# Optimization experiments

Hardware: AMD Instinct MI355X
Metric: run time of the kernel (lower is better)

The kernel has to match this reference:

```python
import jax, jax.numpy as jnp
import numpy as np

S, B, I, H = 2048, 4096, 2, 6  # seq, batch, input_size, hidden_size


def setup_inputs() -> dict:
    key = jax.random.key(0)
    ks = jax.random.split(key, 11)
    init = lambda k, sh: jax.random.normal(k, sh, dtype=jnp.float32) * 0.1
    return {
        "x": jax.random.normal(ks[0], (S, B, I), dtype=jnp.float32),
        # layer-0 LSTM params (PyTorch gate order: i, f, g, o)
        "Wih0": init(ks[1], (4 * H, I)),
        "Whh0": init(ks[2], (4 * H, H)),
        "bih0": init(ks[3], (4 * H,)),
        "bhh0": init(ks[4], (4 * H,)),
        # layer-1 LSTM params
        "Wih1": init(ks[5], (4 * H, H)),
        "Whh1": init(ks[6], (4 * H, H)),
        "bih1": init(ks[7], (4 * H,)),
        "bhh1": init(ks[8], (4 * H,)),
        # final Linear(6, 1)
        "W2": init(ks[9], (1, H)),
        "b2": init(ks[10], (1,)),
    }


def _lstm_layer(x, Wih, Whh, bih, bhh):
    # x: (S, B, in_dim) -> hidden outputs (S, B, H)
    Bn = x.shape[1]
    Hn = Whh.shape[1]
    b = bih + bhh
    # precompute input projections for all timesteps at once (memory-bound GEMM)
    xg = jnp.einsum("sbi,gi->sbg", x, Wih) + b  # (S, B, 4H)

    def step(carry, xt_g):
        h, c = carry
        g = xt_g + h @ Whh.T  # (B, 4H)
        i, f, gg, o = jnp.split(g, 4, axis=-1)
        i = jax.nn.sigmoid(i)
        f = jax.nn.sigmoid(f)
        gg = jnp.tanh(gg)
        o = jax.nn.sigmoid(o)
        c = f * c + i * gg
        h = o * jnp.tanh(c)
        return (h, c), h

    h0 = jnp.zeros((Bn, Hn), dtype=x.dtype)
    c0 = jnp.zeros((Bn, Hn), dtype=x.dtype)
    _, hs = jax.lax.scan(step, (h0, c0), xg)
    return hs  # (S, B, H)


def reference(x, Wih0, Whh0, bih0, bhh0, Wih1, Whh1, bih1, bhh1, W2, b2):
    h1 = _lstm_layer(x, Wih0, Whh0, bih0, bhh0)   # (S, B, H)
    h2 = _lstm_layer(h1, Wih1, Whh1, bih1, bhh1)  # (S, B, H); dropout disabled (eval)
    flat = h2.reshape(-1, H)                       # (S*B, H)
    out = flat @ W2.T + b2                         # (S*B, 1) — original discards final view
    return out
```

## Files before the change

### kernel.cpp

```cpp
#include <hip/hip_runtime.h>

#define SEQ   2048
#define BATCH 4096
#define HID   6
#define BLK   256

typedef float v2f __attribute__((ext_vector_type(2)));
typedef unsigned u2 __attribute__((ext_vector_type(2)));

__device__ __forceinline__ float fexp2(float a) {
#if __has_builtin(__builtin_amdgcn_exp2f)
  return __builtin_amdgcn_exp2f(a);
#else
  float r; asm("v_exp_f32 %0, %1" : "=v"(r) : "v"(a)); return r;
#endif
}
__device__ __forceinline__ float frcp(float a) {
#if __has_builtin(__builtin_amdgcn_rcpf)
  return __builtin_amdgcn_rcpf(a);
#else
  float r; asm("v_rcp_f32 %0, %1" : "=v"(r) : "v"(a)); return r;
#endif
}

template <int CTRL>
__device__ __forceinline__ float dppf(float v) {
  int r = __builtin_amdgcn_update_dpp(0, __builtin_bit_cast(int, v), CTRL, 0xF, 0xF, true);
  return __builtin_bit_cast(float, r);
}

__device__ __forceinline__ float xhalf(float v, bool hi) {
#if __has_builtin(__builtin_amdgcn_permlane32_swap)
  u2 r = __builtin_amdgcn_permlane32_swap(__builtin_bit_cast(unsigned, v),
                                          __builtin_bit_cast(unsigned, v), false, false);
  return __builtin_bit_cast(float, hi ? r.x : r.y);
#else
  unsigned d = __builtin_bit_cast(unsigned, v), s = d;
  asm volatile("v_permlane32_swap_b32 %0, %1" : "+v"(d), "+v"(s));
  return __builtin_bit_cast(float, hi ? d : s);
#endif
}

__global__ __launch_bounds__(BLK, 1) void lstm2_kernel(
    const float* __restrict__ x,
    const float* __restrict__ Wih0, const float* __restrict__ Whh0,
    const float* __restrict__ bih0, const float* __restrict__ bhh0,
    const float* __restrict__ Wih1, const float* __restrict__ Whh1,
    const float* __restrict__ bih1, const float* __restrict__ bhh1,
    const float* __restrict__ W2,   const float* __restrict__ b2,
    float* __restrict__ out)
{
  __shared__ float obuf[64][16];

  const int tid = threadIdx.x;
  const int wib = tid >> 6;
  const int l6  = tid & 63;
  const bool hi = l6 >= 32;
  const int j   = l6 & 31;
  const int el  = j >> 3;
  const int u   = j & 7;
  const int uu  = (u < HID) ? u : (HID - 1);
  const int b   = blockIdx.x * 16 + wib * 4 + el;

  v2f WA[4][4], WB[4][4], w2r[4];
  float BS[4];
#pragma unroll
  for (int q = 0; q < 4; ++q) {
    const int rq = q * HID + uu;
    const float Kq = (q == 2) ? -2.8853900817779268f : -1.4426950408889634f;
#pragma unroll
    for (int k = 0; k < 4; ++k) {
      const int k0 = u ^ (2 * k), k1 = u ^ (2 * k + 1);
      const bool ok0 = (k0 < HID), ok1 = (k1 < HID);
      if (!hi) {
        WA[q][k] = v2f{0.f, 0.f};
        WB[q][k] = v2f{ok0 ? Kq * Whh0[rq * HID + k0] : 0.f,
                       ok1 ? Kq * Whh0[rq * HID + k1] : 0.f};
      } else {
        WA[q][k] = v2f{ok0 ? Kq * Wih1[rq * HID + k0] : 0.f,
                       ok1 ? Kq * Wih1[rq * HID + k1] : 0.f};
        WB[q][k] = v2f{ok0 ? Kq * Whh1[rq * HID + k0] : 0.f,
                       ok1 ? Kq * Whh1[rq * HID + k1] : 0.f};
      }
    }
    if (!hi) WA[q][0] = v2f{Kq * Wih0[rq * 2 + 0], Kq * Wih0[rq * 2 + 1]};
    BS[q] = Kq * ((!hi ? bih0[rq] : bih1[rq]) + (!hi ? bhh0[rq] : bhh1[rq]));
  }
#pragma unroll
  for (int k = 0; k < 4; ++k) {
    const int k0 = u ^ (2 * k), k1 = u ^ (2 * k + 1);
    w2r[k] = v2f{(k0 < HID) ? W2[k0] : 0.f, (k1 < HID) ? W2[k1] : 0.f};
  }
  const float bout = b2[0];
  const float KT = 2.8853900817779268f;

  float h = 0.f, c = 0.f;

  auto gath = [&](float hv, v2f (&g)[4]) {
    float t1 = dppf<0xB1>(hv);
    float t2 = dppf<0x4E>(hv);
    float t3 = dppf<0x4E>(t1);
    float m  = dppf<0x141>(hv);
    float m1 = dppf<0xB1>(m);
    float m2 = dppf<0x4E>(m);
    float m3 = dppf<0x4E>(m1);
    g[0] = v2f{hv, t1};
    g[1] = v2f{t2, t3};
    g[2] = v2f{m3, m2};
    g[3] = v2f{m1, m};
  };

  auto step = [&](v2f xc, float& ov) {
    v2f g2[4]; gath(h, g2);
    float hs = xhalf(h, hi);
    v2f g1[4]; gath(hs, g1);
    v2f v10 = hi ? g1[0] : xc;

    float a[4];
#pragma unroll
    for (int q = 0; q < 4; ++q) {
      v2f accA = __builtin_elementwise_fma(WA[q][0], v10, v2f{BS[q], 0.f});
      accA = __builtin_elementwise_fma(WA[q][1], g1[1], accA);
      accA = __builtin_elementwise_fma(WA[q][2], g1[2], accA);
      accA = __builtin_elementwise_fma(WA[q][3], g1[3], accA);
      v2f accB = WB[q][0] * g2[0];
      accB = __builtin_elementwise_fma(WB[q][1], g2[1], accB);
      accB = __builtin_elementwise_fma(WB[q][2], g2[2], accB);
      accB = __builtin_elementwise_fma(WB[q][3], g2[3], accB);
      v2f acc = accA + accB;
      a[q] = acc.x + acc.y;
    }
    v2f ao = __builtin_elementwise_fma(w2r[0], g2[0],
             __builtin_elementwise_fma(w2r[1], g2[1],
             __builtin_elementwise_fma(w2r[2], g2[2],
             __builtin_elementwise_fma(w2r[3], g2[3], v2f{bout, 0.f}))));
    ov = ao.x + ao.y;

    float i_ = frcp(1.f + fexp2(a[0]));
    float f_ = frcp(1.f + fexp2(a[1]));
    float g_ = fmaf(2.f, frcp(1.f + fexp2(a[2])), -1.f);
    float o_ = frcp(1.f + fexp2(a[3]));
    c = fmaf(f_, c, i_ * g_);
    float th = fmaf(-2.f, frcp(1.f + fexp2(c * KT)), 1.f);
    h = o_ * th;
  };

  auto flush = [&](int rbase) {
    const int r = tid >> 2, jj = (tid & 3) * 4;
    float4 vv = *(const float4*)&obuf[r][jj];
    *(float4*)&out[(size_t)(rbase + r) * BATCH + blockIdx.x * 16 + jj] = vv;
  };

  const v2f* x2 = (const v2f*)x;
  v2f xc  = x2[(size_t)0 * BATCH + b];
  v2f xn1 = x2[(size_t)1 * BATCH + b];
  v2f xn2 = x2[(size_t)2 * BATCH + b];
  v2f xn3 = x2[(size_t)3 * BATCH + b];

  {
    float ov;
    step(xc, ov);
    if (hi) { h = 0.f; c = 0.f; }
    v2f xf = x2[(size_t)4 * BATCH + b];
    xc = xn1; xn1 = xn2; xn2 = xn3; xn3 = xf;
  }

#pragma unroll 1
  for (int t = 1; t < SEQ; ++t) {
    int tf = t + 4; tf = (tf < SEQ) ? tf : (SEQ - 1);
    v2f xf = x2[(size_t)tf * BATCH + b];

    float ov;
    step(xc, ov);

    if (t >= 2) {
      const int r = t - 2;
      if (hi && u == 0) obuf[r & 63][wib * 4 + el] = ov;
      if ((r & 63) == 63) {
        __syncthreads();
        flush(r - 63);
        __syncthreads();
      }
    }
    xc = xn1; xn1 = xn2; xn2 = xn3; xn3 = xf;
  }

  {
    float ov;
    step(xc, ov);
    if (hi && u == 0) obuf[62][wib * 4 + el] = ov;
    v2f g2[4]; gath(h, g2);
    v2f ao = __builtin_elementwise_fma(w2r[0], g2[0],
             __builtin_elementwise_fma(w2r[1], g2[1],
             __builtin_elementwise_fma(w2r[2], g2[2],
             __builtin_elementwise_fma(w2r[3], g2[3], v2f{bout, 0.f}))));
    if (hi && u == 0) obuf[63][wib * 4 + el] = ao.x + ao.y;
    __syncthreads();
    flush(SEQ - 64);
  }
}

extern "C" void kernel_launch(void* const* d_in, const int* in_sizes, int n_in,
                              void* d_out, int out_size, void* d_ws, size_t ws_size,
                              hipStream_t stream) {
  const float* x    = (const float*)d_in[0];
  const float* Wih0 = (const float*)d_in[1];
  const float* Whh0 = (const float*)d_in[2];
  const float* bih0 = (const float*)d_in[3];
  const float* bhh0 = (const float*)d_in[4];
  const float* Wih1 = (const float*)d_in[5];
  const float* Whh1 = (const float*)d_in[6];
  const float* bih1 = (const float*)d_in[7];
  const float* bhh1 = (const float*)d_in[8];
  const float* W2   = (const float*)d_in[9];
  const float* b2   = (const float*)d_in[10];
  float* out = (float*)d_out;

  dim3 grid(BATCH / 16);
  dim3 block(BLK);
  hipLaunchKernelGGL(lstm2_kernel, grid, block, 0, stream,
                     x, Wih0, Whh0, bih0, bhh0, Wih1, Whh1, bih1, bhh1, W2, b2, out);
}
```

Baseline: 651.4 us.

## Split LSTM layers across waves with LDS ring handoff and staged x tiles

Layer 0 and layer 1 move to separate wavefronts. Before, they were the lower and upper halves of each wave, and the layer-1 input was exchanged with permlane32_swap. Now wave 0 runs layer 0 and writes h into a double-buffered LDS ring. Wave 1 reads that ring one step later to run layer 1 and the output projection. Input x is staged in 64-step LDS tiles with asynchronous-style prefetch, and blocks now hold 8 batch elements with 128 threads, doubling the grid. The cost is a __syncthreads every timestep, which may add latency to the serial recurrence.

```diff
diff --git a/kernel.cpp b/kernel.cpp
--- a/kernel.cpp
+++ b/kernel.cpp
@@ -3,10 +3,9 @@
 #define SEQ   2048
 #define BATCH 4096
 #define HID   6
-#define BLK   256
+#define BLK   128
 
 typedef float v2f __attribute__((ext_vector_type(2)));
-typedef unsigned u2 __attribute__((ext_vector_type(2)));
 
 __device__ __forceinline__ float fexp2(float a) {
 #if __has_builtin(__builtin_amdgcn_exp2f)
@@ -27,18 +26,6 @@
 __device__ __forceinline__ float dppf(float v) {
   int r = __builtin_amdgcn_update_dpp(0, __builtin_bit_cast(int, v), CTRL, 0xF, 0xF, true);
   return __builtin_bit_cast(float, r);
-}
-
-__device__ __forceinline__ float xhalf(float v, bool hi) {
-#if __has_builtin(__builtin_amdgcn_permlane32_swap)
-  u2 r = __builtin_amdgcn_permlane32_swap(__builtin_bit_cast(unsigned, v),
-                                          __builtin_bit_cast(unsigned, v), false, false);
-  return __builtin_bit_cast(float, hi ? r.x : r.y);
-#else
-  unsigned d = __builtin_bit_cast(unsigned, v), s = d;
-  asm volatile("v_permlane32_swap_b32 %0, %1" : "+v"(d), "+v"(s));
-  return __builtin_bit_cast(float, hi ? d : s);
-#endif
 }
 
 __global__ __launch_bounds__(BLK, 1) void lstm2_kernel(
@@ -50,41 +37,46 @@
     const float* __restrict__ W2,   const float* __restrict__ b2,
     float* __restrict__ out)
 {
-  __shared__ float obuf[64][16];
+  __shared__ float xbuf[2][64][16];
+  __shared__ float obuf[64][8];
+  __shared__ float ring[2][8][8];
 
   const int tid = threadIdx.x;
   const int wib = tid >> 6;
   const int l6  = tid & 63;
-  const bool hi = l6 >= 32;
-  const int j   = l6 & 31;
-  const int el  = j >> 3;
-  const int u   = j & 7;
+  const int el  = l6 >> 3;
+  const int u   = l6 & 7;
   const int uu  = (u < HID) ? u : (HID - 1);
-  const int b   = blockIdx.x * 16 + wib * 4 + el;
-
-  v2f WA[4][4], WB[4][4], w2r[4];
+
+  v2f WIN[4][3], WRr[4][4], w2r[4];
   float BS[4];
 #pragma unroll
   for (int q = 0; q < 4; ++q) {
     const int rq = q * HID + uu;
     const float Kq = (q == 2) ? -2.8853900817779268f : -1.4426950408889634f;
-#pragma unroll
-    for (int k = 0; k < 4; ++k) {
-      const int k0 = u ^ (2 * k), k1 = u ^ (2 * k + 1);
-      const bool ok0 = (k0 < HID), ok1 = (k1 < HID);
-      if (!hi) {
-        WA[q][k] = v2f{0.f, 0.f};
-        WB[q][k] = v2f{ok0 ? Kq * Whh0[rq * HID + k0] : 0.f,
-                       ok1 ? Kq * Whh0[rq * HID + k1] : 0.f};
-      } else {
-        WA[q][k] = v2f{ok0 ? Kq * Wih1[rq * HID + k0] : 0.f,
-                       ok1 ? Kq * Wih1[rq * HID + k1] : 0.f};
-        WB[q][k] = v2f{ok0 ? Kq * Whh1[rq * HID + k0] : 0.f,
-                       ok1 ? Kq * Whh1[rq * HID + k1] : 0.f};
-      }
-    }
-    if (!hi) WA[q][0] = v2f{Kq * Wih0[rq * 2 + 0], Kq * Wih0[rq * 2 + 1]};
-    BS[q] = Kq * ((!hi ? bih0[rq] : bih1[rq]) + (!hi ? bhh0[rq] : bhh1[rq]));
+    if (wib == 0) {
+      WIN[q][0] = v2f{Kq * Wih0[rq * 2 + 0], Kq * Wih0[rq * 2 + 1]};
+      WIN[q][1] = v2f{0.f, 0.f};
+      WIN[q][2] = v2f{0.f, 0.f};
+#pragma unroll
+      for (int k = 0; k < 4; ++k) {
+        const int k0 = u ^ (2 * k), k1 = u ^ (2 * k + 1);
+        WRr[q][k] = v2f{(k0 < HID) ? Kq * Whh0[rq * HID + k0] : 0.f,
+                        (k1 < HID) ? Kq * Whh0[rq * HID + k1] : 0.f};
+      }
+      BS[q] = Kq * (bih0[rq] + bhh0[rq]);
+    } else {
+#pragma unroll
+      for (int k = 0; k < 3; ++k)
+        WIN[q][k] = v2f{Kq * Wih1[rq * HID + 2 * k], Kq * Wih1[rq * HID + 2 * k + 1]};
+#pragma unroll
+      for (int k = 0; k < 4; ++k) {
+        const int k0 = u ^ (2 * k), k1 = u ^ (2 * k + 1);
+        WRr[q][k] = v2f{(k0 < HID) ? Kq * Whh1[rq * HID + k0] : 0.f,
+                        (k1 < HID) ? Kq * Whh1[rq * HID + k1] : 0.f};
+      }
+      BS[q] = Kq * (bih1[rq] + bhh1[rq]);
+    }
   }
 #pragma unroll
   for (int k = 0; k < 4; ++k) {
@@ -110,32 +102,20 @@
     g[3] = v2f{m1, m};
   };
 
-  auto step = [&](v2f xc, float& ov) {
-    v2f g2[4]; gath(h, g2);
-    float hs = xhalf(h, hi);
-    v2f g1[4]; gath(hs, g1);
-    v2f v10 = hi ? g1[0] : xc;
-
+  auto cell = [&](v2f in0, v2f in1, v2f in2, v2f (&g)[4]) {
+    gath(h, g);
     float a[4];
 #pragma unroll
     for (int q = 0; q < 4; ++q) {
-      v2f accA = __builtin_elementwise_fma(WA[q][0], v10, v2f{BS[q], 0.f});
-      accA = __builtin_elementwise_fma(WA[q][1], g1[1], accA);
-      accA = __builtin_elementwise_fma(WA[q][2], g1[2], accA);
-      accA = __builtin_elementwise_fma(WA[q][3], g1[3], accA);
-      v2f accB = WB[q][0] * g2[0];
-      accB = __builtin_elementwise_fma(WB[q][1], g2[1], accB);
-      accB = __builtin_elementwise_fma(WB[q][2], g2[2], accB);
-      accB = __builtin_elementwise_fma(WB[q][3], g2[3], accB);
-      v2f acc = accA + accB;
+      v2f acc = __builtin_elementwise_fma(WIN[q][0], in0, v2f{BS[q], 0.f});
+      acc = __builtin_elementwise_fma(WIN[q][1], in1, acc);
+      acc = __builtin_elementwise_fma(WIN[q][2], in2, acc);
+      acc = __builtin_elementwise_fma(WRr[q][0], g[0], acc);
+      acc = __builtin_elementwise_fma(WRr[q][1], g[1], acc);
+      acc = __builtin_elementwise_fma(WRr[q][2], g[2], acc);
+      acc = __builtin_elementwise_fma(WRr[q][3], g[3], acc);
       a[q] = acc.x + acc.y;
     }
-    v2f ao = __builtin_elementwise_fma(w2r[0], g2[0],
-             __builtin_elementwise_fma(w2r[1], g2[1],
-             __builtin_elementwise_fma(w2r[2], g2[2],
-             __builtin_elementwise_fma(w2r[3], g2[3], v2f{bout, 0.f}))));
-    ov = ao.x + ao.y;
-
     float i_ = frcp(1.f + fexp2(a[0]));
     float f_ = frcp(1.f + fexp2(a[1]));
     float g_ = fmaf(2.f, frcp(1.f + fexp2(a[2])), -1.f);
@@ -145,59 +125,98 @@
     h = o_ * th;
   };
 
+  auto outdot = [&](const v2f (&g)[4]) -> float {
+    v2f ao = __builtin_elementwise_fma(w2r[0], g[0],
+             __builtin_elementwise_fma(w2r[1], g[1],
+             __builtin_elementwise_fma(w2r[2], g[2],
+             __builtin_elementwise_fma(w2r[3], g[3], v2f{bout, 0.f}))));
+    return ao.x + ao.y;
+  };
+
   auto flush = [&](int rbase) {
-    const int r = tid >> 2, jj = (tid & 3) * 4;
-    float4 vv = *(const float4*)&obuf[r][jj];
-    *(float4*)&out[(size_t)(rbase + r) * BATCH + blockIdx.x * 16 + jj] = vv;
-  };
-
-  const v2f* x2 = (const v2f*)x;
-  v2f xc  = x2[(size_t)0 * BATCH + b];
-  v2f xn1 = x2[(size_t)1 * BATCH + b];
-  v2f xn2 = x2[(size_t)2 * BATCH + b];
-  v2f xn3 = x2[(size_t)3 * BATCH + b];
+    const int r = tid >> 1, off = (tid & 1) * 4;
+    float4 vv = *(const float4*)&obuf[r][off];
+    *(float4*)&out[(size_t)(rbase + r) * BATCH + blockIdx.x * 8 + off] = vv;
+  };
 
   {
-    float ov;
-    step(xc, ov);
-    if (hi) { h = 0.f; c = 0.f; }
-    v2f xf = x2[(size_t)4 * BATCH + b];
-    xc = xn1; xn1 = xn2; xn2 = xn3; xn3 = xf;
+    const int row = tid >> 1, off = (tid & 1) * 8;
+    const float* s0 = x + (size_t)row * (BATCH * 2) + blockIdx.x * 16 + off;
+    const float* s1 = s0 + (size_t)64 * (BATCH * 2);
+    float4 a0 = *(const float4*)s0, a1 = *(const float4*)(s0 + 4);
+    float4 b0 = *(const float4*)s1, b1 = *(const float4*)(s1 + 4);
+    *(float4*)&xbuf[0][row][off]     = a0;
+    *(float4*)&xbuf[0][row][off + 4] = a1;
+    *(float4*)&xbuf[1][row][off]     = b0;
+    *(float4*)&xbuf[1][row][off + 4] = b1;
+    __syncthreads();
+  }
+
+  const v2f Z = v2f{0.f, 0.f};
+  v2f xr = *(const v2f*)&xbuf[0][0][el * 2];
+
+  {
+    v2f g[4];
+    cell(wib ? Z : xr, Z, Z, g);
+    if (wib) { h = 0.f; c = 0.f; }
+    else if (u < HID) ring[0][el][u] = h;
+    xr = *(const v2f*)&xbuf[0][1][el * 2];
+    __syncthreads();
   }
 
 #pragma unroll 1
   for (int t = 1; t < SEQ; ++t) {
-    int tf = t + 4; tf = (tf < SEQ) ? tf : (SEQ - 1);
-    v2f xf = x2[(size_t)tf * BATCH + b];
-
-    float ov;
-    step(xc, ov);
-
-    if (t >= 2) {
-      const int r = t - 2;
-      if (hi && u == 0) obuf[r & 63][wib * 4 + el] = ov;
-      if ((r & 63) == 63) {
-        __syncthreads();
-        flush(r - 63);
-        __syncthreads();
-      }
-    }
-    xc = xn1; xn1 = xn2; xn2 = xn3; xn3 = xf;
-  }
-
-  {
-    float ov;
-    step(xc, ov);
-    if (hi && u == 0) obuf[62][wib * 4 + el] = ov;
+    v2f hp0 = Z, hp1 = Z, hp2 = Z, xnew = xr;
+    if (wib) {
+      const v2f* hp = (const v2f*)&ring[(t - 1) & 1][el][0];
+      hp0 = hp[0]; hp1 = hp[1]; hp2 = hp[2];
+    } else {
+      const int tn = (t + 1 < SEQ) ? t + 1 : SEQ - 1;
+      xnew = *(const v2f*)&xbuf[(tn >> 6) & 1][tn & 63][el * 2];
+    }
+
+    v2f g[4];
+    cell(wib ? hp0 : xr, hp1, hp2, g);
+
+    if (wib) {
+      if (t >= 2 && u == 0) obuf[(t - 2) & 63][el] = outdot(g);
+    } else {
+      if (u < HID) ring[t & 1][el][u] = h;
+    }
+
+    if (t >= 2 && ((t - 2) & 63) == 63) {
+      const int ck = (t >> 6) + 1;
+      const bool doR = (ck * 64 < SEQ);
+      const int row = tid >> 1, off = (tid & 1) * 8;
+      float4 r0, r1;
+      if (doR) {
+        const float* src = x + ((size_t)(ck * 64) + row) * (BATCH * 2)
+                             + blockIdx.x * 16 + off;
+        r0 = *(const float4*)src;
+        r1 = *(const float4*)(src + 4);
+      }
+      __syncthreads();
+      flush(t - 2 - 63);
+      if (doR) {
+        *(float4*)&xbuf[ck & 1][row][off]     = r0;
+        *(float4*)&xbuf[ck & 1][row][off + 4] = r1;
+      }
+    }
+    __syncthreads();
+    xr = xnew;
+  }
+
+  if (wib) {
+    const v2f* hp = (const v2f*)&ring[(SEQ - 1) & 1][el][0];
+    v2f hp0 = hp[0], hp1 = hp[1], hp2 = hp[2];
+    v2f g[4];
+    cell(hp0, hp1, hp2, g);
+    if (u == 0) obuf[62][el] = outdot(g);
     v2f g2[4]; gath(h, g2);
-    v2f ao = __builtin_elementwise_fma(w2r[0], g2[0],
-             __builtin_elementwise_fma(w2r[1], g2[1],
-             __builtin_elementwise_fma(w2r[2], g2[2],
-             __builtin_elementwise_fma(w2r[3], g2[3], v2f{bout, 0.f}))));
-    if (hi && u == 0) obuf[63][wib * 4 + el] = ao.x + ao.y;
-    __syncthreads();
-    flush(SEQ - 64);
-  }
+    if (u == 0) obuf[63][el] = outdot(g2);
+  }
+  __syncthreads();
+  flush(SEQ - 64);
 }
 
 extern "C" void kernel_launch(void* const* d_in, const int* in_sizes, int n_in,
@@ -216,7 +235,7 @@
   const float* b2   = (const float*)d_in[10];
   float* out = (float*)d_out;
 
-  dim3 grid(BATCH / 16);
+  dim3 grid(BATCH / 8);
   dim3 block(BLK);
   hipLaunchKernelGGL(lstm2_kernel, grid, block, 0, stream,
                      x, Wih0, Whh0, bih0, bhh0, Wih1, Whh1, bih1, bhh1, W2, b2, out);
```

After: 819.6 us. 1.26x slower.
